# Kernel optimization log

Measured on AMD Instinct MI355X. Metric: run time of the kernel, lower is better.

Reference implementation:

```python
import jax, jax.numpy as jnp
import numpy as np

B, T, IN, UNITS, BB, NC = 1024, 2048, 4, 256, 128, 10


def lecun_tanh(x):
    return 1.7159 * jnp.tanh(0.666 * x)


def setup_inputs() -> dict:
    key = jax.random.key(0)
    ks = jax.random.split(key, 8)
    g = lambda k, shape, s: (jax.random.normal(k, shape, jnp.float32) * s)
    return {
        "x": jax.random.normal(ks[0], (B, T, IN), jnp.float32),
        # backbone: Linear(IN+UNITS -> BB) + lecun_tanh
        "W_bb": g(ks[1], (IN + UNITS, BB), 0.06),
        "b_bb": jnp.zeros((BB,), jnp.float32),
        # CfC heads: ff1, ff2, time_a, time_b : Linear(BB -> UNITS)
        "W_ff1": g(ks[2], (BB, UNITS), 0.09),
        "b_ff1": jnp.zeros((UNITS,), jnp.float32),
        "W_ff2": g(ks[3], (BB, UNITS), 0.09),
        "b_ff2": jnp.zeros((UNITS,), jnp.float32),
        "W_ta": g(ks[4], (BB, UNITS), 0.09),
        "b_ta": jnp.zeros((UNITS,), jnp.float32),
        "W_tb": g(ks[5], (BB, UNITS), 0.09),
        "b_tb": jnp.zeros((UNITS,), jnp.float32),
        # output projection: Linear(UNITS -> NC)
        "W_fc": g(ks[6], (UNITS, NC), 0.06),
        "b_fc": jnp.zeros((NC,), jnp.float32),
    }


def reference(x, W_bb, b_bb, W_ff1, b_ff1, W_ff2, b_ff2, W_ta, b_ta, W_tb, b_tb, W_fc, b_fc):
    # CfC (mode='default', backbone_layers=1, ts=1.0), batch_first, then mean over time.
    batch = x.shape[0]
    units = W_ff1.shape[1]
    h0 = jnp.zeros((batch, units), x.dtype)
    xs = jnp.swapaxes(x, 0, 1)  # [T, B, IN]

    def step(h, xt):
        z = jnp.concatenate([xt, h], axis=-1)          # [B, IN+UNITS]
        bb = lecun_tanh(z @ W_bb + b_bb)               # [B, BB]
        ff1 = jnp.tanh(bb @ W_ff1 + b_ff1)             # [B, UNITS]
        ff2 = jnp.tanh(bb @ W_ff2 + b_ff2)
        # ts = 1.0 -> sigmoid(time_a * 1.0 + time_b)
        t_interp = jax.nn.sigmoid((bb @ W_ta + b_ta) + (bb @ W_tb + b_tb))
        h_new = ff1 * (1.0 - t_interp) + t_interp * ff2
        out_t = h_new @ W_fc + b_fc                    # [B, NC]
        return h_new, out_t

    _, outs = jax.lax.scan(step, h0, xs)               # outs: [T, B, NC]
    return jnp.mean(outs, axis=0)                      # torch.mean(out, dim=1)
```

## Files before the change

kernel.cpp:

```cpp
#include <hip/hip_runtime.h>

#define Tq     2048
#define INq    4
#define UNITSq 256
#define BBq    128
#define NCq    10
#define HBS    288
#define BBS    160

typedef __bf16 bf16x8 __attribute__((ext_vector_type(8)));
typedef float  f32x4  __attribute__((ext_vector_type(4)));
typedef float  f32x2  __attribute__((ext_vector_type(2)));

__device__ __forceinline__ float rcpf(float x) { return __builtin_amdgcn_rcpf(x); }
__device__ __forceinline__ float tanh_f(float x) {
    float e = __expf(x + x);
    return 1.0f - 2.0f * rcpf(e + 1.0f);
}
__device__ __forceinline__ float lecun_f(float x) {
    float e = __expf(1.332f * x);
    return 1.7159f - 3.4318f * rcpf(e + 1.0f);
}
__device__ __forceinline__ float sigm_f(float x) {
    return rcpf(1.0f + __expf(-x));
}
__device__ __forceinline__ float sel4(f32x4 v, int i) {
    float lo = (i & 1) ? v[1] : v[0];
    float hi = (i & 1) ? v[3] : v[2];
    return (i & 2) ? hi : lo;
}

__global__ __launch_bounds__(512, 2) void cfc_kernel(
    const float* __restrict__ x,
    const float* __restrict__ W_bb, const float* __restrict__ b_bb,
    const float* __restrict__ W_ff1, const float* __restrict__ b_ff1,
    const float* __restrict__ W_ff2, const float* __restrict__ b_ff2,
    const float* __restrict__ W_ta, const float* __restrict__ b_ta,
    const float* __restrict__ W_tb, const float* __restrict__ b_tb,
    const float* __restrict__ W_fc, const float* __restrict__ b_fc,
    float* __restrict__ out)
{
    const int tid = threadIdx.x;
    const int w   = tid >> 6;
    const int l   = tid & 63;
    const int l4  = l >> 4;
    const int lc  = l & 15;
    const int bbase = blockIdx.x * 4;

    __shared__ __bf16 hb[4 * HBS];
    __shared__ __bf16 bbuf[4 * BBS];
    __shared__ float  xstage[2][512];
    __shared__ float  hsum_lds[4][256];

    bf16x8 WH[3][2][4];
    #pragma unroll
    for (int tl = 0; tl < 2; ++tl) {
        const int u = w * 32 + 2 * lc + tl;
        #pragma unroll
        for (int kt = 0; kt < 4; ++kt) {
            bf16x8 f1, f2, ts;
            #pragma unroll
            for (int j = 0; j < 8; ++j) {
                const int k = kt * 32 + l4 * 8 + j;
                f1[j] = (__bf16)W_ff1[k * UNITSq + u];
                f2[j] = (__bf16)W_ff2[k * UNITSq + u];
                ts[j] = (__bf16)(W_ta[k * UNITSq + u] + W_tb[k * UNITSq + u]);
            }
            WH[0][tl][kt] = f1; WH[1][tl][kt] = f2; WH[2][tl][kt] = ts;
        }
    }
    const int cb = w * 16 + lc;
    bf16x8 WB[9];
    #pragma unroll
    for (int kt = 0; kt < 8; ++kt) {
        bf16x8 f;
        #pragma unroll
        for (int j = 0; j < 8; ++j) {
            const int k = kt * 32 + l4 * 8 + j;
            f[j] = (__bf16)W_bb[(4 + k) * BBq + cb];
        }
        WB[kt] = f;
    }
    {
        bf16x8 f;
        #pragma unroll
        for (int j = 0; j < 8; ++j) {
            const int k = l4 * 8 + j;
            f[j] = (k < 4) ? (__bf16)W_bb[k * BBq + cb] : (__bf16)0.0f;
        }
        WB[8] = f;
    }
    const float bias_bb_r = b_bb[cb];
    const int ru0 = w * 32 + 2 * lc;
    const float bf1a = b_ff1[ru0], bf1b = b_ff1[ru0 + 1];
    const float bf2a = b_ff2[ru0], bf2b = b_ff2[ru0 + 1];
    const float bta_ = b_ta[ru0] + b_tb[ru0];
    const float btb_ = b_ta[ru0 + 1] + b_tb[ru0 + 1];

    for (int i = tid; i < 4 * HBS; i += 512) hb[i] = (__bf16)0.0f;
    {
        const int r = tid >> 7, off = tid & 127;
        xstage[0][r * 128 + off] = x[((size_t)(bbase + r) * Tq + (off >> 2)) * INq + (off & 3)];
    }
    float xv;
    {
        const int r = tid >> 7, off = tid & 127;
        xv = x[((size_t)(bbase + r) * Tq + 32 + (off >> 2)) * INq + (off & 3)];
    }
    if (tid < 16) {
        const int r = tid >> 2, q = tid & 3;
        hb[r * HBS + 256 + q] = (__bf16)x[((size_t)(bbase + r) * Tq + 0) * INq + q];
    }
    __syncthreads();

    float hsumA = 0.f, hsumB = 0.f;
    const int rowc = lc & 3;

    for (int t = 0; t < Tq; ++t) {
        float xnew = 0.f;
        if ((t & 31) == 0) {
            const int r = tid >> 7, off = tid & 127;
            int tel = t + 64 + (off >> 2);
            tel = (tel < Tq) ? tel : (Tq - 1);
            xnew = x[((size_t)(bbase + r) * Tq + tel) * INq + (off & 3)];
        }

        f32x4 p0 = {0.f,0.f,0.f,0.f}, p1 = {0.f,0.f,0.f,0.f};
        f32x4 p2 = {0.f,0.f,0.f,0.f}, p3 = {0.f,0.f,0.f,0.f};
        #pragma unroll
        for (int kt = 0; kt < 9; ++kt) {
            bf16x8 a = *(const bf16x8*)&hb[rowc * HBS + kt * 32 + l4 * 8];
            switch (kt & 3) {
                case 0: p0 = __builtin_amdgcn_mfma_f32_16x16x32_bf16(a, WB[kt], p0, 0, 0, 0); break;
                case 1: p1 = __builtin_amdgcn_mfma_f32_16x16x32_bf16(a, WB[kt], p1, 0, 0, 0); break;
                case 2: p2 = __builtin_amdgcn_mfma_f32_16x16x32_bf16(a, WB[kt], p2, 0, 0, 0); break;
                case 3: p3 = __builtin_amdgcn_mfma_f32_16x16x32_bf16(a, WB[kt], p3, 0, 0, 0); break;
            }
        }
        {
            f32x4 s = (p0 + p1) + (p2 + p3);
            float pre = sel4(s, l4) + bias_bb_r;
            bbuf[l4 * BBS + cb] = (__bf16)lecun_f(pre);
        }
        __syncthreads();

        f32x4 acc[3][2] = {};
        #pragma unroll
        for (int kt = 0; kt < 4; ++kt) {
            bf16x8 a = *(const bf16x8*)&bbuf[rowc * BBS + kt * 32 + l4 * 8];
            #pragma unroll
            for (int hh = 0; hh < 3; ++hh)
                #pragma unroll
                for (int tl = 0; tl < 2; ++tl)
                    acc[hh][tl] = __builtin_amdgcn_mfma_f32_16x16x32_bf16(a, WH[hh][tl][kt], acc[hh][tl], 0, 0, 0);
        }
        {
            float f1a = tanh_f(sel4(acc[0][0], l4) + bf1a);
            float f1b = tanh_f(sel4(acc[0][1], l4) + bf1b);
            float f2a = tanh_f(sel4(acc[1][0], l4) + bf2a);
            float f2b = tanh_f(sel4(acc[1][1], l4) + bf2b);
            float tta = sigm_f(sel4(acc[2][0], l4) + bta_);
            float ttb = sigm_f(sel4(acc[2][1], l4) + btb_);
            float ha  = f1a + tta * (f2a - f1a);
            float hbv = f1b + ttb * (f2b - f1b);
            hsumA += ha; hsumB += hbv;
            union { __bf16 b[2]; unsigned int u; } pk;
            pk.b[0] = (__bf16)ha; pk.b[1] = (__bf16)hbv;
            *(unsigned int*)&hb[l4 * HBS + ru0] = pk.u;
        }
        if (w == 7 && l < 16 && t + 1 < Tq) {
            const int r = l >> 2, q = l & 3;
            const int tn = t + 1;
            hb[r * HBS + 256 + q] = (__bf16)xstage[(tn >> 5) & 1][r * 128 + (tn & 31) * 4 + q];
        }
        if ((t & 31) == 0) {
            const int r = tid >> 7, off = tid & 127;
            xstage[((t >> 5) + 1) & 1][r * 128 + off] = xv;
            xv = xnew;
        }
        __syncthreads();
    }

    *(f32x2*)&hsum_lds[l4][ru0] = (f32x2){hsumA, hsumB};
    __syncthreads();
    if (w == 0 && l < 40) {
        const int r = l / 10, c = l % 10;
        float s = 0.f;
        #pragma unroll 8
        for (int u = 0; u < 256; ++u)
            s += hsum_lds[r][u] * W_fc[u * NCq + c];
        out[(bbase + r) * NCq + c] = s * (1.0f / Tq) + b_fc[c];
    }
}

extern "C" void kernel_launch(void* const* d_in, const int* in_sizes, int n_in,
                              void* d_out, int out_size, void* d_ws, size_t ws_size,
                              hipStream_t stream) {
    const float* x     = (const float*)d_in[0];
    const float* W_bb  = (const float*)d_in[1];
    const float* b_bb  = (const float*)d_in[2];
    const float* W_ff1 = (const float*)d_in[3];
    const float* b_ff1 = (const float*)d_in[4];
    const float* W_ff2 = (const float*)d_in[5];
    const float* b_ff2 = (const float*)d_in[6];
    const float* W_ta  = (const float*)d_in[7];
    const float* b_ta  = (const float*)d_in[8];
    const float* W_tb  = (const float*)d_in[9];
    const float* b_tb  = (const float*)d_in[10];
    const float* W_fc  = (const float*)d_in[11];
    const float* b_fc  = (const float*)d_in[12];
    float* out = (float*)d_out;

    hipLaunchKernelGGL(cfc_kernel, dim3(256), dim3(512), 0, stream,
                       x, W_bb, b_bb, W_ff1, b_ff1, W_ff2, b_ff2,
                       W_ta, b_ta, W_tb, b_tb, W_fc, b_fc, out);
}
```

Before: 1.950 ms.

## Interleave two independent batch groups to overlap recurrent stages

Splits each block's four batch rows into two independent groups (A and B) with separate LDS buffers, and staggers them so one group's head matmul runs alongside the other group's backbone matmul between barriers. Each 4-row MFMA tile now carries only two live rows per group, so the MFMA work per time step doubles while the dependent chain gets hidden. This trades redundant padded MFMA work for the chance to overlap the two dependent phases per barrier.

```diff
diff --git a/kernel.cpp b/kernel.cpp
--- a/kernel.cpp
+++ b/kernel.cpp
@@ -47,8 +47,8 @@
     const int lc  = l & 15;
     const int bbase = blockIdx.x * 4;
 
-    __shared__ __bf16 hb[4 * HBS];
-    __shared__ __bf16 bbuf[4 * BBS];
+    __shared__ __bf16 hbA[4 * HBS], hbB[4 * HBS];
+    __shared__ __bf16 bbA[4 * BBS], bbB[4 * BBS];
     __shared__ float  xstage[2][512];
     __shared__ float  hsum_lds[4][256];
 
@@ -97,7 +97,7 @@
     const float bta_ = b_ta[ru0] + b_tb[ru0];
     const float btb_ = b_ta[ru0 + 1] + b_tb[ru0 + 1];
 
-    for (int i = tid; i < 4 * HBS; i += 512) hb[i] = (__bf16)0.0f;
+    for (int i = tid; i < 4 * HBS; i += 512) { hbA[i] = (__bf16)0.0f; hbB[i] = (__bf16)0.0f; }
     {
         const int r = tid >> 7, off = tid & 127;
         xstage[0][r * 128 + off] = x[((size_t)(bbase + r) * Tq + (off >> 2)) * INq + (off & 3)];
@@ -107,16 +107,64 @@
         const int r = tid >> 7, off = tid & 127;
         xv = x[((size_t)(bbase + r) * Tq + 32 + (off >> 2)) * INq + (off & 3)];
     }
-    if (tid < 16) {
-        const int r = tid >> 2, q = tid & 3;
-        hb[r * HBS + 256 + q] = (__bf16)x[((size_t)(bbase + r) * Tq + 0) * INq + q];
-    }
-    __syncthreads();
-
-    float hsumA = 0.f, hsumB = 0.f;
+    if (tid < 32) {
+        const int cB = tid >> 4;
+        const int r4 = (tid & 15) >> 2, q = tid & 3;
+        const float v = x[((size_t)(bbase + cB * 2 + (r4 & 1)) * Tq + 0) * INq + q];
+        (cB ? hbB : hbA)[r4 * HBS + 256 + q] = (__bf16)v;
+    }
+    __syncthreads();
+
+    float hsA0 = 0.f, hsA1 = 0.f, hsB0 = 0.f, hsB1 = 0.f;
     const int rowc = lc & 3;
 
-    for (int t = 0; t < Tq; ++t) {
+    auto P0 = [&](const __bf16* __restrict__ hbc, __bf16* __restrict__ bbc) {
+        f32x4 p0 = {0.f,0.f,0.f,0.f}, p1 = {0.f,0.f,0.f,0.f};
+        f32x4 p2 = {0.f,0.f,0.f,0.f}, p3 = {0.f,0.f,0.f,0.f};
+        #pragma unroll
+        for (int kt = 0; kt < 9; ++kt) {
+            bf16x8 a = *(const bf16x8*)&hbc[rowc * HBS + kt * 32 + l4 * 8];
+            switch (kt & 3) {
+                case 0: p0 = __builtin_amdgcn_mfma_f32_16x16x32_bf16(a, WB[kt], p0, 0, 0, 0); break;
+                case 1: p1 = __builtin_amdgcn_mfma_f32_16x16x32_bf16(a, WB[kt], p1, 0, 0, 0); break;
+                case 2: p2 = __builtin_amdgcn_mfma_f32_16x16x32_bf16(a, WB[kt], p2, 0, 0, 0); break;
+                case 3: p3 = __builtin_amdgcn_mfma_f32_16x16x32_bf16(a, WB[kt], p3, 0, 0, 0); break;
+            }
+        }
+        f32x4 s = (p0 + p1) + (p2 + p3);
+        float pre = sel4(s, l4) + bias_bb_r;
+        bbc[l4 * BBS + cb] = (__bf16)lecun_f(pre);
+    };
+    auto P1 = [&](const __bf16* __restrict__ bbc, __bf16* __restrict__ hbc,
+                  float& s0, float& s1) {
+        f32x4 acc[3][2] = {};
+        #pragma unroll
+        for (int kt = 0; kt < 4; ++kt) {
+            bf16x8 a = *(const bf16x8*)&bbc[rowc * BBS + kt * 32 + l4 * 8];
+            #pragma unroll
+            for (int hh = 0; hh < 3; ++hh)
+                #pragma unroll
+                for (int tl = 0; tl < 2; ++tl)
+                    acc[hh][tl] = __builtin_amdgcn_mfma_f32_16x16x32_bf16(a, WH[hh][tl][kt], acc[hh][tl], 0, 0, 0);
+        }
+        float f1a = tanh_f(sel4(acc[0][0], l4) + bf1a);
+        float f1b = tanh_f(sel4(acc[0][1], l4) + bf1b);
+        float f2a = tanh_f(sel4(acc[1][0], l4) + bf2a);
+        float f2b = tanh_f(sel4(acc[1][1], l4) + bf2b);
+        float tta = sigm_f(sel4(acc[2][0], l4) + bta_);
+        float ttb = sigm_f(sel4(acc[2][1], l4) + btb_);
+        float ha  = f1a + tta * (f2a - f1a);
+        float hbv = f1b + ttb * (f2b - f1b);
+        s0 += ha; s1 += hbv;
+        union { __bf16 b[2]; unsigned int u; } pk;
+        pk.b[0] = (__bf16)ha; pk.b[1] = (__bf16)hbv;
+        *(unsigned int*)&hbc[l4 * HBS + ru0] = pk.u;
+    };
+
+    P0(hbA, bbA);
+    __syncthreads();
+
+    for (int t = 0; t < Tq - 1; ++t) {
         float xnew = 0.f;
         if ((t & 31) == 0) {
             const int r = tid >> 7, off = tid & 127;
@@ -124,54 +172,20 @@
             tel = (tel < Tq) ? tel : (Tq - 1);
             xnew = x[((size_t)(bbase + r) * Tq + tel) * INq + (off & 3)];
         }
-
-        f32x4 p0 = {0.f,0.f,0.f,0.f}, p1 = {0.f,0.f,0.f,0.f};
-        f32x4 p2 = {0.f,0.f,0.f,0.f}, p3 = {0.f,0.f,0.f,0.f};
-        #pragma unroll
-        for (int kt = 0; kt < 9; ++kt) {
-            bf16x8 a = *(const bf16x8*)&hb[rowc * HBS + kt * 32 + l4 * 8];
-            switch (kt & 3) {
-                case 0: p0 = __builtin_amdgcn_mfma_f32_16x16x32_bf16(a, WB[kt], p0, 0, 0, 0); break;
-                case 1: p1 = __builtin_amdgcn_mfma_f32_16x16x32_bf16(a, WB[kt], p1, 0, 0, 0); break;
-                case 2: p2 = __builtin_amdgcn_mfma_f32_16x16x32_bf16(a, WB[kt], p2, 0, 0, 0); break;
-                case 3: p3 = __builtin_amdgcn_mfma_f32_16x16x32_bf16(a, WB[kt], p3, 0, 0, 0); break;
-            }
-        }
-        {
-            f32x4 s = (p0 + p1) + (p2 + p3);
-            float pre = sel4(s, l4) + bias_bb_r;
-            bbuf[l4 * BBS + cb] = (__bf16)lecun_f(pre);
+        P1(bbA, hbA, hsA0, hsA1);
+        P0(hbB, bbB);
+        if (w == 7 && l < 16) {
+            const int r4 = l >> 2, q = l & 3, tn = t + 1;
+            hbA[r4 * HBS + 256 + q] =
+                (__bf16)xstage[(tn >> 5) & 1][(r4 & 1) * 128 + (tn & 31) * 4 + q];
         }
         __syncthreads();
-
-        f32x4 acc[3][2] = {};
-        #pragma unroll
-        for (int kt = 0; kt < 4; ++kt) {
-            bf16x8 a = *(const bf16x8*)&bbuf[rowc * BBS + kt * 32 + l4 * 8];
-            #pragma unroll
-            for (int hh = 0; hh < 3; ++hh)
-                #pragma unroll
-                for (int tl = 0; tl < 2; ++tl)
-                    acc[hh][tl] = __builtin_amdgcn_mfma_f32_16x16x32_bf16(a, WH[hh][tl][kt], acc[hh][tl], 0, 0, 0);
-        }
-        {
-            float f1a = tanh_f(sel4(acc[0][0], l4) + bf1a);
-            float f1b = tanh_f(sel4(acc[0][1], l4) + bf1b);
-            float f2a = tanh_f(sel4(acc[1][0], l4) + bf2a);
-            float f2b = tanh_f(sel4(acc[1][1], l4) + bf2b);
-            float tta = sigm_f(sel4(acc[2][0], l4) + bta_);
-            float ttb = sigm_f(sel4(acc[2][1], l4) + btb_);
-            float ha  = f1a + tta * (f2a - f1a);
-            float hbv = f1b + ttb * (f2b - f1b);
-            hsumA += ha; hsumB += hbv;
-            union { __bf16 b[2]; unsigned int u; } pk;
-            pk.b[0] = (__bf16)ha; pk.b[1] = (__bf16)hbv;
-            *(unsigned int*)&hb[l4 * HBS + ru0] = pk.u;
-        }
-        if (w == 7 && l < 16 && t + 1 < Tq) {
-            const int r = l >> 2, q = l & 3;
-            const int tn = t + 1;
-            hb[r * HBS + 256 + q] = (__bf16)xstage[(tn >> 5) & 1][r * 128 + (tn & 31) * 4 + q];
+        P0(hbA, bbA);
+        P1(bbB, hbB, hsB0, hsB1);
+        if (w == 6 && l < 16) {
+            const int r4 = l >> 2, q = l & 3, tn = t + 1;
+            hbB[r4 * HBS + 256 + q] =
+                (__bf16)xstage[(tn >> 5) & 1][(2 + (r4 & 1)) * 128 + (tn & 31) * 4 + q];
         }
         if ((t & 31) == 0) {
             const int r = tid >> 7, off = tid & 127;
@@ -180,8 +194,15 @@
         }
         __syncthreads();
     }
-
-    *(f32x2*)&hsum_lds[l4][ru0] = (f32x2){hsumA, hsumB};
+    P1(bbA, hbA, hsA0, hsA1);
+    P0(hbB, bbB);
+    __syncthreads();
+    P1(bbB, hbB, hsB0, hsB1);
+
+    if (l4 < 2) {
+        *(f32x2*)&hsum_lds[l4][ru0]     = (f32x2){hsA0, hsA1};
+        *(f32x2*)&hsum_lds[2 + l4][ru0] = (f32x2){hsB0, hsB1};
+    }
     __syncthreads();
     if (w == 0 && l < 40) {
         const int r = l / 10, c = l % 10;
```

Measured after the change: 3.569 ms. 83.0% more time.

## Split time loop into chunks, use LDS-only barriers and MFMA priority hints

Applied to the files above, without the earlier changes.

Restructures the time loop into 64 chunks of 32 steps and moves the x prefetch and staging store to chunk boundaries. __syncthreads is replaced with a barrier that waits only on LDS counters, so the outstanding global x load no longer stalls every step. It also wraps the MFMA sections in s_setprio and cuts the backbone accumulators from four to two chains. The risk is shorter MFMA dependency chains and a subtle hazard in the staging order: the xstage write at chunk start now sits right after the previous step's barrier, with no barrier before it.

```diff
diff --git a/kernel.cpp b/kernel.cpp
--- a/kernel.cpp
+++ b/kernel.cpp
@@ -28,6 +28,13 @@
     float lo = (i & 1) ? v[1] : v[0];
     float hi = (i & 1) ? v[3] : v[2];
     return (i & 2) ? hi : lo;
+}
+
+__device__ __forceinline__ void bar_lds() {
+    __builtin_amdgcn_sched_barrier(0);
+    asm volatile("s_waitcnt lgkmcnt(0)" ::: "memory");
+    __builtin_amdgcn_s_barrier();
+    __builtin_amdgcn_sched_barrier(0);
 }
 
 __global__ __launch_bounds__(512, 2) void cfc_kernel(
@@ -116,69 +123,68 @@
     float hsumA = 0.f, hsumB = 0.f;
     const int rowc = lc & 3;
 
-    for (int t = 0; t < Tq; ++t) {
-        float xnew = 0.f;
-        if ((t & 31) == 0) {
+    for (int c = 0; c < 64; ++c) {
+        {
             const int r = tid >> 7, off = tid & 127;
-            int tel = t + 64 + (off >> 2);
+            xstage[(c + 1) & 1][r * 128 + off] = xv;
+            int tel = c * 32 + 64 + (off >> 2);
             tel = (tel < Tq) ? tel : (Tq - 1);
-            xnew = x[((size_t)(bbase + r) * Tq + tel) * INq + (off & 3)];
-        }
-
-        f32x4 p0 = {0.f,0.f,0.f,0.f}, p1 = {0.f,0.f,0.f,0.f};
-        f32x4 p2 = {0.f,0.f,0.f,0.f}, p3 = {0.f,0.f,0.f,0.f};
-        #pragma unroll
-        for (int kt = 0; kt < 9; ++kt) {
-            bf16x8 a = *(const bf16x8*)&hb[rowc * HBS + kt * 32 + l4 * 8];
-            switch (kt & 3) {
-                case 0: p0 = __builtin_amdgcn_mfma_f32_16x16x32_bf16(a, WB[kt], p0, 0, 0, 0); break;
-                case 1: p1 = __builtin_amdgcn_mfma_f32_16x16x32_bf16(a, WB[kt], p1, 0, 0, 0); break;
-                case 2: p2 = __builtin_amdgcn_mfma_f32_16x16x32_bf16(a, WB[kt], p2, 0, 0, 0); break;
-                case 3: p3 = __builtin_amdgcn_mfma_f32_16x16x32_bf16(a, WB[kt], p3, 0, 0, 0); break;
-            }
-        }
-        {
-            f32x4 s = (p0 + p1) + (p2 + p3);
-            float pre = sel4(s, l4) + bias_bb_r;
-            bbuf[l4 * BBS + cb] = (__bf16)lecun_f(pre);
-        }
-        __syncthreads();
-
-        f32x4 acc[3][2] = {};
-        #pragma unroll
-        for (int kt = 0; kt < 4; ++kt) {
-            bf16x8 a = *(const bf16x8*)&bbuf[rowc * BBS + kt * 32 + l4 * 8];
+            xv = x[((size_t)(bbase + r) * Tq + tel) * INq + (off & 3)];
+        }
+
+        for (int i = 0; i < 32; ++i) {
+            const int t = c * 32 + i;
+
+            f32x4 p0 = {0.f,0.f,0.f,0.f}, p1 = {0.f,0.f,0.f,0.f};
+            __builtin_amdgcn_s_setprio(1);
             #pragma unroll
-            for (int hh = 0; hh < 3; ++hh)
+            for (int kt = 0; kt < 9; ++kt) {
+                bf16x8 a = *(const bf16x8*)&hb[rowc * HBS + kt * 32 + l4 * 8];
+                if (kt & 1) p1 = __builtin_amdgcn_mfma_f32_16x16x32_bf16(a, WB[kt], p1, 0, 0, 0);
+                else        p0 = __builtin_amdgcn_mfma_f32_16x16x32_bf16(a, WB[kt], p0, 0, 0, 0);
+            }
+            __builtin_amdgcn_s_setprio(0);
+            {
+                f32x4 s = p0 + p1;
+                float pre = sel4(s, l4) + bias_bb_r;
+                bbuf[l4 * BBS + cb] = (__bf16)lecun_f(pre);
+            }
+            bar_lds();
+
+            f32x4 acc[3][2] = {};
+            __builtin_amdgcn_s_setprio(1);
+            #pragma unroll
+            for (int kt = 0; kt < 4; ++kt) {
+                bf16x8 a = *(const bf16x8*)&bbuf[rowc * BBS + kt * 32 + l4 * 8];
                 #pragma unroll
-                for (int tl = 0; tl < 2; ++tl)
-                    acc[hh][tl] = __builtin_amdgcn_mfma_f32_16x16x32_bf16(a, WH[hh][tl][kt], acc[hh][tl], 0, 0, 0);
-        }
-        {
-            float f1a = tanh_f(sel4(acc[0][0], l4) + bf1a);
-            float f1b = tanh_f(sel4(acc[0][1], l4) + bf1b);
-            float f2a = tanh_f(sel4(acc[1][0], l4) + bf2a);
-            float f2b = tanh_f(sel4(acc[1][1], l4) + bf2b);
-            float tta = sigm_f(sel4(acc[2][0], l4) + bta_);
-            float ttb = sigm_f(sel4(acc[2][1], l4) + btb_);
-            float ha  = f1a + tta * (f2a - f1a);
-            float hbv = f1b + ttb * (f2b - f1b);
-            hsumA += ha; hsumB += hbv;
-            union { __bf16 b[2]; unsigned int u; } pk;
-            pk.b[0] = (__bf16)ha; pk.b[1] = (__bf16)hbv;
-            *(unsigned int*)&hb[l4 * HBS + ru0] = pk.u;
-        }
-        if (w == 7 && l < 16 && t + 1 < Tq) {
-            const int r = l >> 2, q = l & 3;
-            const int tn = t + 1;
-            hb[r * HBS + 256 + q] = (__bf16)xstage[(tn >> 5) & 1][r * 128 + (tn & 31) * 4 + q];
-        }
-        if ((t & 31) == 0) {
-            const int r = tid >> 7, off = tid & 127;
-            xstage[((t >> 5) + 1) & 1][r * 128 + off] = xv;
-            xv = xnew;
-        }
-        __syncthreads();
+                for (int hh = 0; hh < 3; ++hh)
+                    #pragma unroll
+                    for (int tl = 0; tl < 2; ++tl)
+                        acc[hh][tl] = __builtin_amdgcn_mfma_f32_16x16x32_bf16(a, WH[hh][tl][kt], acc[hh][tl], 0, 0, 0);
+            }
+            __builtin_amdgcn_s_setprio(0);
+            {
+                float f1a = tanh_f(sel4(acc[0][0], l4) + bf1a);
+                float f1b = tanh_f(sel4(acc[0][1], l4) + bf1b);
+                float f2a = tanh_f(sel4(acc[1][0], l4) + bf2a);
+                float f2b = tanh_f(sel4(acc[1][1], l4) + bf2b);
+                float tta = sigm_f(sel4(acc[2][0], l4) + bta_);
+                float ttb = sigm_f(sel4(acc[2][1], l4) + btb_);
+                float ha  = f1a + tta * (f2a - f1a);
+                float hbv = f1b + ttb * (f2b - f1b);
+                hsumA += ha; hsumB += hbv;
+                union { __bf16 b[2]; unsigned int u; } pk;
+                pk.b[0] = (__bf16)ha; pk.b[1] = (__bf16)hbv;
+                *(unsigned int*)&hb[l4 * HBS + ru0] = pk.u;
+            }
+            if (w == 7 && l < 16 && t + 1 < Tq) {
+                const int r = l >> 2, q = l & 3;
+                const int tn = t + 1;
+                hb[r * HBS + 256 + q] =
+                    (__bf16)xstage[(tn >> 5) & 1][r * 128 + (tn & 31) * 4 + q];
+            }
+            bar_lds();
+        }
     }
 
     *(f32x2*)&hsum_lds[l4][ru0] = (f32x2){hsumA, hsumB};
```

Result: faster. 1.825 ms (-6.4%).
